# Kernel tuning notes

Measured on AMD Instinct MI355X. Metric: run time of the kernel, lower is better.

The kernel has to match this reference:

```python
import jax, jax.numpy as jnp
import numpy as np

B, N, ND_, FEAT, WV = 32, 1024, 8, 2048, 300
E, T, STEPS = 20000, 2, 5
NDIM = N * ND_  # 8192


def setup_inputs() -> dict:
    key = jax.random.key(0)
    ks = jax.random.split(key, 20)
    s = 0.02
    inputs = jax.random.normal(ks[0], (B, FEAT), jnp.float32)
    wordvecs = jax.random.normal(ks[1], (N, WV), jnp.float32)
    # unique edges per type (disjoint across types) so the scatter has no duplicate indices
    rng = np.random.default_rng(0)
    codes = rng.permutation(N * N)[: T * E].reshape(T, E)
    edge_u = (codes // N).astype(np.int32)
    edge_v = (codes % N).astype(np.int32)
    ki = np.repeat(np.arange(ND_), ND_)
    kj = np.tile(np.arange(ND_), ND_)
    mat_u = (edge_u.reshape(-1)[:, None] * ND_ + ki[None, :]).reshape(-1).astype(np.int32)
    mat_v = (edge_v.reshape(-1)[:, None] * ND_ + kj[None, :]).reshape(-1).astype(np.int32)
    p = {
        'inputs': inputs, 'wordvecs': wordvecs,
        'edge_u': jnp.asarray(edge_u), 'edge_v': jnp.asarray(edge_v),
        'mat_u': jnp.asarray(mat_u), 'mat_v': jnp.asarray(mat_v),
        # Inputnet: Linear(feat+wv -> 512), Linear(512 -> node_dim)
        'W_in1': jax.random.normal(ks[2], (512, FEAT + WV), jnp.float32) * s,
        'b_in1': jnp.zeros((512,), jnp.float32),
        'W_in2': jax.random.normal(ks[3], (ND_, 512), jnp.float32) * s,
        'b_in2': jnp.zeros((ND_,), jnp.float32),
        # embnet: Linear(wv -> 50)
        'W_emb': jax.random.normal(ks[4], (50, WV), jnp.float32) * s,
        'b_emb': jnp.zeros((50,), jnp.float32),
        # relnets: one (50, 50*nd^2) matrix per edge type
        'rel_mats': jax.random.normal(ks[5], (T, 50, 50 * ND_ * ND_), jnp.float32) * s,
        # GRUCell(node_dim, node_dim)
        'W_ih': jax.random.normal(ks[6], (3 * ND_, ND_), jnp.float32) * s,
        'W_hh': jax.random.normal(ks[7], (3 * ND_, ND_), jnp.float32) * s,
        'b_ih': jnp.zeros((3 * ND_,), jnp.float32),
        'b_hh': jnp.zeros((3 * ND_,), jnp.float32),
        # outnet: Linear(nd -> 20), ReLU, Linear(20 -> 1)
        'W_o1': jax.random.normal(ks[8], (20, ND_), jnp.float32) * s,
        'b_o1': jnp.zeros((20,), jnp.float32),
        'W_o2': jax.random.normal(ks[9], (1, 20), jnp.float32) * s,
        'b_o2': jnp.zeros((1,), jnp.float32),
    }
    return p


def reference(inputs, wordvecs, edge_u, edge_v, mat_u, mat_v,
              W_in1, b_in1, W_in2, b_in2, W_emb, b_emb, rel_mats,
              W_ih, W_hh, b_ih, b_hh, W_o1, b_o1, W_o2, b_o2):
    nd = W_in2.shape[0]
    n_nodes = wordvecs.shape[0]
    ndim = n_nodes * nd
    bsz = inputs.shape[0]

    # Inputnet: per-(image, node) feature -> initial hidden state [B, N*nd]
    f = jnp.concatenate([
        jnp.broadcast_to(inputs[:, None, :], (bsz, n_nodes, inputs.shape[1])),
        jnp.broadcast_to(wordvecs[None, :, :], (bsz, n_nodes, wordvecs.shape[1])),
    ], axis=-1).reshape(bsz * n_nodes, -1)
    h = jax.nn.relu(f @ W_in1.T + b_in1) @ W_in2.T + b_in2  # [B*N, nd]
    hidden = h.reshape(bsz, ndim)

    # edge weights via Relnet per edge type
    embs = wordvecs @ W_emb.T + b_emb  # [N, 50]
    ws = []
    for t in range(rel_mats.shape[0]):
        ue = embs[edge_u[t]]  # [E, 50]
        ve = embs[edge_v[t]]  # [E, 50]
        tmp = (ue @ rel_mats[t]).reshape(ue.shape[0], embs.shape[1], nd * nd)
        ws.append(jnp.einsum('ed,edk->ek', ve, tmp))  # [E, nd^2]
    weights = jnp.concatenate(ws, axis=0).reshape(-1)

    # scatter into dense propagation matrix
    P = jnp.zeros((ndim, ndim), jnp.float32).at[mat_u, mat_v].set(weights)
    norm = jnp.sqrt(jnp.sum(P * P, axis=1))  # row L2 norms [ndim]
    norm = norm + (norm == 0).astype(P.dtype)
    P = P / norm  # NOTE: torch broadcasting divides COLUMNS by row norms (faithful)

    def gru(x, hc):
        gi = x @ W_ih.T + b_ih
        gh = hc @ W_hh.T + b_hh
        ir, iz, inn = jnp.split(gi, 3, axis=-1)
        hr, hz, hn = jnp.split(gh, 3, axis=-1)
        r = jax.nn.sigmoid(ir + hr)
        z = jax.nn.sigmoid(iz + hz)
        n = jnp.tanh(inn + r * hn)
        return (1.0 - z) * n + z * hc

    hiddens = [hidden]
    for _ in range(STEPS):
        x = jnp.tanh(hidden @ P.T)  # [B, ndim]
        hidden = gru(x.reshape(-1, nd), hidden.reshape(-1, nd)).reshape(bsz, ndim)
        hiddens.append(hidden)
    states = jnp.stack(hiddens, axis=1)  # [B, STEPS+1, ndim]

    o = jax.nn.relu(states.reshape(-1, nd) @ W_o1.T + b_o1) @ W_o2.T + b_o2  # [B*(S+1)*N, 1]
    logits = o.reshape(bsz, STEPS + 1, n_nodes).transpose(0, 2, 1)  # [B, N, S+1]
    return logits
```

## Files before the change

kernel.cpp:

```cpp
#include <hip/hip_runtime.h>
#include <math.h>

constexpr int B = 32, N = 1024, ND = 8, FEAT = 2048, WVD = 300;
constexpr int E = 20000, T = 2, STEPS = 5;
constexpr int NDIM = N * ND;
constexpr int H1 = 512;
constexpr int W1C = FEAT + WVD;
constexpr int EMB = 50;
constexpr int RC = EMB * ND * ND;
constexpr int KH = 150;
constexpr int CAP = 64;
constexpr int SEG = 50;
constexpr int SEGLEN = E / SEG;

constexpr int G_KA   = 512;
constexpr int G_W1T  = 16 * 10;
constexpr int G_EMB  = N * 25 / 4;
constexpr int G_SEGH = T * N * SEG / 4;
constexpr int F1_TOT = G_KA + G_W1T + G_EMB + G_SEGH;

constexpr int G_ARED = 8;
constexpr int G_WV   = 512;
constexpr int G_AHAT = 13 * 32 * T;
constexpr int F2_TOT = G_ARED + G_WV + G_AHAT;

constexpr int G_INP  = N / 4;
constexpr int F3_TOT = N + G_INP;

__global__ __launch_bounds__(256) void k_f1(
        const int* eu, int* segcnt,
        const float* inp, const float* W1, float* partA, float* W1T,
        const float* wv, const float* We, const float* be,
        float* embs, float* embsT) {
    __shared__ float smem[8 * 260];
    int tid = threadIdx.x;
    int blk = blockIdx.x;
    if (blk < G_KA) {
        int c = tid & 7, b = tid >> 3;
        int c0 = (blk & 63) * 8;
        int ks = blk >> 6;
        int kt = ks * 256;
        {
            int r = tid >> 5, cb = (tid & 31) * 8;
            const float* src = W1 + (size_t)(c0 + r) * W1C + kt + cb;
            float4 a0 = *(const float4*)src;
            float4 a1 = *(const float4*)(src + 4);
            *(float4*)&smem[r * 260 + cb] = a0;
            *(float4*)&smem[r * 260 + cb + 4] = a1;
        }
        __syncthreads();
        const float* xr = inp + (size_t)b * FEAT + kt;
        float acc = 0.f;
#pragma unroll 8
        for (int k4 = 0; k4 < 64; k4++) {
            float4 x = *(const float4*)(xr + k4 * 4);
            float4 w = *(const float4*)&smem[c * 260 + k4 * 4];
            acc += x.x * w.x + x.y * w.y + x.z * w.z + x.w * w.w;
        }
        partA[(size_t)ks * (H1 * B) + (c0 + c) * B + b] = acc;
    } else if (blk < G_KA + G_W1T) {
        int lb = blk - G_KA;
        int c0 = (lb % 16) * 32, k0 = (lb / 16) * 32;
        float (*tile)[33] = (float(*)[33])smem;
        int kl = tid & 31, cl4 = tid >> 5;
#pragma unroll
        for (int p = 0; p < 4; p++) {
            int c = cl4 + p * 8;
            int k = k0 + kl;
            if (k < WVD) tile[c][kl] = W1[(size_t)(c0 + c) * W1C + FEAT + k];
        }
        __syncthreads();
        int cl = tid & 31, kl4 = tid >> 5;
#pragma unroll
        for (int p = 0; p < 4; p++) {
            int kk = kl4 + p * 8;
            int k = k0 + kk;
            if (k < WVD) W1T[(size_t)k * H1 + c0 + cl] = tile[cl][kk];
        }
    } else if (blk < G_KA + G_W1T + G_EMB) {
        int lb = blk - G_KA - G_W1T;
        int wid = lb * 4 + (tid >> 6);
        int lane = tid & 63;
        int n = wid / 25, cp = wid - n * 25;
        int c0 = cp * 2;
        const float* xr = wv + (size_t)n * WVD;
        const float* wr0 = We + (size_t)c0 * WVD;
        const float* wr1 = wr0 + WVD;
        float a0 = 0.f, a1 = 0.f;
#pragma unroll
        for (int i = 0; i < 5; i++) {
            int k = i * 64 + lane;
            if (k < WVD) {
                float x = xr[k];
                a0 += x * wr0[k];
                a1 += x * wr1[k];
            }
        }
        for (int m = 32; m; m >>= 1) {
            a0 += __shfl_xor(a0, m, 64);
            a1 += __shfl_xor(a1, m, 64);
        }
        if (lane == 0) {
            float v0 = a0 + be[c0], v1 = a1 + be[c0 + 1];
            embs[n * EMB + c0] = v0;
            embs[n * EMB + c0 + 1] = v1;
            embsT[c0 * N + n] = v0;
            embsT[(c0 + 1) * N + n] = v1;
        }
    } else {
        int lb = blk - G_KA - G_W1T - G_EMB;
        int wid = lb * 4 + (tid >> 6);
        int lane = tid & 63;
        int t = wid / (N * SEG);
        int rem = wid - t * (N * SEG);
        int u = rem / SEG, seg = rem - u * SEG;
        const int* eut = eu + t * E;
        int e0 = seg * SEGLEN, e1 = e0 + SEGLEN, cnt = 0;
        for (int c = e0; c < e1; c += 64) {
            int e = c + lane;
            bool ok = (e < e1) && (eut[e] == u);
            cnt += __popcll(__ballot(ok));
        }
        if (lane == 0) segcnt[(t * N + u) * SEG + seg] = cnt;
    }
}

__global__ __launch_bounds__(256) void k_f2(
        const float* partA, float* AbT,
        const float* wv, const float* W1T, float* Wp,
        const float* embsT, const float* RMbase, float* Ahat) {
    __shared__ float smemf[1800];
    int tid = threadIdx.x, blk = blockIdx.x;
    if (blk < G_ARED) {
        int cb = blk * 2048 + tid * 8;
        float4 s0 = {0, 0, 0, 0}, s1 = {0, 0, 0, 0};
#pragma unroll
        for (int ks = 0; ks < 8; ks++) {
            const float* p = partA + (size_t)ks * (H1 * B) + cb;
            float4 a = *(const float4*)p;
            float4 b4 = *(const float4*)(p + 4);
            s0.x += a.x; s0.y += a.y; s0.z += a.z; s0.w += a.w;
            s1.x += b4.x; s1.y += b4.y; s1.z += b4.z; s1.w += b4.w;
        }
        *(float4*)(AbT + cb) = s0;
        *(float4*)(AbT + cb + 4) = s1;
    } else if (blk < G_ARED + G_WV) {
        int lb = blk - G_ARED;
        int kh = lb >> 8;
        int rem = lb & 255;
        int c = (rem & 1) * 256 + tid;
        int n0 = (rem >> 1) * 8;
        int kb = kh * KH;
        float (*el)[8] = (float(*)[8])smemf;
        for (int idx = tid; idx < 8 * KH; idx += 256) {
            int j = idx / KH, k = idx - j * KH;
            el[k][j] = wv[(size_t)(n0 + j) * WVD + kb + k];
        }
        __syncthreads();
        float acc[8] = {};
#pragma unroll 5
        for (int k = 0; k < KH; k++) {
            float r = W1T[(size_t)(kb + k) * H1 + c];
            float4 e0 = *(const float4*)&el[k][0];
            float4 e1 = *(const float4*)&el[k][4];
            acc[0] += e0.x * r; acc[1] += e0.y * r;
            acc[2] += e0.z * r; acc[3] += e0.w * r;
            acc[4] += e1.x * r; acc[5] += e1.y * r;
            acc[6] += e1.z * r; acc[7] += e1.w * r;
        }
        float* wout = Wp + (size_t)kh * N * H1;
#pragma unroll
        for (int j = 0; j < 8; j++) wout[(size_t)(n0 + j) * H1 + c] = acc[j];
    } else {
        int lb = blk - G_ARED - G_WV;
        int t = lb / 416, r = lb % 416;
        int bx = r % 13, by = r / 13;
        const float* RM = RMbase + (size_t)t * EMB * RC;
        float* Ah = Ahat + (size_t)t * N * RC;
        int n0 = by * 32;
        float (*el)[36] = (float(*)[36])smemf;
        for (int idx = tid; idx < EMB * 32; idx += 256)
            el[idx >> 5][idx & 31] = embsT[(idx >> 5) * N + n0 + (idx & 31)];
        __syncthreads();
        int mi = bx * 256 + (tid & 63) * 4;
        int ni = (tid >> 6) * 8;
        if (mi < RC) {
            float acc[8][4] = {};
#pragma unroll 2
            for (int c = 0; c < EMB; c++) {
                float4 rm = *(const float4*)(RM + (size_t)c * RC + mi);
                float4 e0 = *(const float4*)&el[c][ni];
                float4 e1 = *(const float4*)&el[c][ni + 4];
                float ev[8] = {e0.x, e0.y, e0.z, e0.w, e1.x, e1.y, e1.z, e1.w};
#pragma unroll
                for (int j = 0; j < 8; j++) {
                    acc[j][0] += ev[j] * rm.x;
                    acc[j][1] += ev[j] * rm.y;
                    acc[j][2] += ev[j] * rm.z;
                    acc[j][3] += ev[j] * rm.w;
                }
            }
#pragma unroll
            for (int j = 0; j < 8; j++) {
                float4 o = {acc[j][0], acc[j][1], acc[j][2], acc[j][3]};
                *(float4*)(Ah + (size_t)(n0 + ni + j) * RC + mi) = o;
            }
        }
    }
}

__global__ __launch_bounds__(256) void k_f3(
        const int* eu, const int* ev, const int* segcnt,
        const float* embs, const float* Ahat, float* wbuf, float* inorm,
        int* counts, int* sv,
        const float* AbT, const float* Wp, const float* b1,
        const float* W2, const float* b2, float* sT0) {
    __shared__ float smem[6656];
    int tid = threadIdx.x;
    int blk = blockIdx.x;
    if (blk < N) {
        int u = blk;
        float* AL   = smem;
        int* vl     = (int*)(smem + 3328);
        int* scnt   = vl + T * CAP;
        int* soff   = scnt + T * SEG;
        int* slist  = soff + T * SEG;
        int* smeta  = slist + T * SEG;
        int w = tid >> 6, lane = tid & 63;
        if (tid < T * SEG) {
            int t = tid / SEG, s = tid - t * SEG;
            scnt[tid] = segcnt[((size_t)t * N + u) * SEG + s];
        }
        __syncthreads();
        if (w < T && lane == 0) {
            int off = 0, nn = 0;
            for (int j = 0; j < SEG; j++) {
                int c = scnt[w * SEG + j];
                soff[w * SEG + j] = off;
                off += c;
                if (c > 0) slist[w * SEG + nn++] = j;
            }
            smeta[w] = nn;
            smeta[T + w] = off;
            counts[w * N + u] = off;
        }
        __syncthreads();
        {
            int myrow = w >> 1, sub = w & 1;
            int row = myrow * N + u;
            const int* eut = eu + myrow * E;
            const int* evt = ev + myrow * E;
            int nnz = smeta[myrow];
            for (int idx = sub; idx < nnz; idx += 2) {
                int seg = slist[myrow * SEG + idx];
                int base = soff[myrow * SEG + seg];
                int e0 = seg * SEGLEN, e1 = e0 + SEGLEN, cnt = 0;
                for (int c = e0; c < e1; c += 64) {
                    int e = c + lane;
                    bool ok = (e < e1) && (eut[e] == u);
                    unsigned long long m = __ballot(ok);
                    if (ok) {
                        int rank = __popcll(m & ((1ull << lane) - 1));
                        int pos = base + cnt + rank;
                        vl[myrow * CAP + pos] = evt[e];
                        sv[(size_t)row * CAP + pos] = evt[e];
                    }
                    cnt += __popcll(m);
                }
            }
        }
        __syncthreads();
        int cnts[T];
#pragma unroll
        for (int t = 0; t < T; t++) cnts[t] = smeta[T + t];
        int k = lane;
        float ssq = 0.f;
        for (int t = 0; t < T; t++) {
            __syncthreads();
            for (int idx = tid; idx < RC; idx += 256)
                AL[idx] = Ahat[((size_t)t * N + u) * RC + idx];
            __syncthreads();
            int cnt = cnts[t];
            size_t base = (size_t)(t * N + u) * CAP;
            for (int i = w; i < cnt; i += 4) {
                int v = vl[t * CAP + i];
                const float* vr = embs + v * EMB;
                float acc = 0.f;
#pragma unroll 10
                for (int d = 0; d < EMB; d++) acc += vr[d] * AL[d * 64 + k];
                wbuf[(base + i) * 64 + k] = acc;
                ssq += acc * acc;
            }
        }
        __syncthreads();
        AL[w * 64 + k] = ssq;
        __syncthreads();
        if (tid < 64) {
            float tot = AL[tid] + AL[64 + tid] + AL[128 + tid] + AL[192 + tid];
            tot += __shfl_xor(tot, 1, 64);
            tot += __shfl_xor(tot, 2, 64);
            tot += __shfl_xor(tot, 4, 64);
            int ki = tid >> 3, kj = tid & 7;
            if (kj == 0) {
                float nv = sqrtf(tot);
                if (nv == 0.f) nv = 1.f;
                inorm[u * ND + ki] = 1.0f / nv;
            }
        }
    } else {
        int n0 = (blk - N) * 4;
        float* w2s  = smem;
        float* wvs  = smem + 4096;
        float* part = smem + 4608;
        for (int idx = tid; idx < 8 * H1; idx += 256) w2s[idx] = W2[idx];
        int b = tid & 31, s = tid >> 5;
        int ki2 = tid >> 5, b2i = tid & 31;
        for (int nn = 0; nn < 4; nn++) {
            int n = n0 + nn;
            __syncthreads();
            for (int idx = tid; idx < H1; idx += 256)
                wvs[idx] = Wp[(size_t)n * H1 + idx]
                         + Wp[(size_t)N * H1 + (size_t)n * H1 + idx] + b1[idx];
            __syncthreads();
            float acc[8] = {};
            for (int i = 0; i < 64; i++) {
                int c = s * 64 + i;
                float tv = fmaxf(AbT[c * 32 + b] + wvs[c], 0.f);
#pragma unroll
                for (int ki = 0; ki < 8; ki++) acc[ki] += tv * w2s[ki * H1 + c];
            }
#pragma unroll
            for (int ki = 0; ki < 8; ki++) part[s * 256 + ki * 32 + b] = acc[ki];
            __syncthreads();
            float tot = b2[ki2];
#pragma unroll
            for (int s2 = 0; s2 < 8; s2++) tot += part[s2 * 256 + ki2 * 32 + b2i];
            sT0[(size_t)n * 256 + tid] = tot;
        }
    }
}

__global__ __launch_bounds__(256) void k_step(
        const int* counts, const int* sv,
        const float* wbuf, const float* inorm, const float* sT, int s,
        const float* W_ih, const float* W_hh, const float* b_ih, const float* b_hh,
        const float* Wo1, const float* bo1, const float* Wo2, const float* bo2,
        float* sOut, float* out, int last) {
    __shared__ float xs[256], hs[256], hfin[256];
    __shared__ float wih[192], whh[192];
    __shared__ float w1s[160], b1s[20], w2s[20];
    __shared__ float res[8][33];
    int tid = threadIdx.x;
    int u = blockIdx.x;
    int ki = tid >> 5, b = tid & 31;
    if (tid < 192) { wih[tid] = W_ih[tid]; whh[tid] = W_hh[tid]; }
    if (last) {
        if (tid < 160) w1s[tid] = Wo1[tid];
        if (tid < 20) { b1s[tid] = bo1[tid]; w2s[tid] = Wo2[tid]; }
    }
    const float* sIn = sT + (size_t)s * NDIM * B;
    float hown = sIn[((size_t)u * 8 + ki) * B + b];
    float acc = 0.f;
    for (int t = 0; t < T; t++) {
        int row = t * N + u;
        int cnt = counts[row];
        size_t base = (size_t)row * CAP;
        int i = 0;
        for (; i + 1 < cnt; i += 2) {
            size_t s0 = base + i, s1 = base + i + 1;
            int v0 = sv[s0], v1 = sv[s1];
            const float* wp0 = wbuf + s0 * 64 + ki * 8;
            const float* wp1 = wbuf + s1 * 64 + ki * 8;
            float4 wa0 = *(const float4*)wp0;
            float4 wb0 = *(const float4*)(wp0 + 4);
            float4 wa1 = *(const float4*)wp1;
            float4 wb1 = *(const float4*)(wp1 + 4);
            const float* ip0 = inorm + v0 * ND;
            const float* ip1 = inorm + v1 * ND;
            const float* hp0 = sIn + (size_t)v0 * 256 + b;
            const float* hp1 = sIn + (size_t)v1 * 256 + b;
            acc += (wa0.x * ip0[0]) * hp0[0]   + (wa0.y * ip0[1]) * hp0[32]
                 + (wa0.z * ip0[2]) * hp0[64]  + (wa0.w * ip0[3]) * hp0[96]
                 + (wb0.x * ip0[4]) * hp0[128] + (wb0.y * ip0[5]) * hp0[160]
                 + (wb0.z * ip0[6]) * hp0[192] + (wb0.w * ip0[7]) * hp0[224];
            acc += (wa1.x * ip1[0]) * hp1[0]   + (wa1.y * ip1[1]) * hp1[32]
                 + (wa1.z * ip1[2]) * hp1[64]  + (wa1.w * ip1[3]) * hp1[96]
                 + (wb1.x * ip1[4]) * hp1[128] + (wb1.y * ip1[5]) * hp1[160]
                 + (wb1.z * ip1[6]) * hp1[192] + (wb1.w * ip1[7]) * hp1[224];
        }
        if (i < cnt) {
            size_t s0 = base + i;
            int v0 = sv[s0];
            const float* wp0 = wbuf + s0 * 64 + ki * 8;
            float4 wa0 = *(const float4*)wp0;
            float4 wb0 = *(const float4*)(wp0 + 4);
            const float* ip0 = inorm + v0 * ND;
            const float* hp0 = sIn + (size_t)v0 * 256 + b;
            acc += (wa0.x * ip0[0]) * hp0[0]   + (wa0.y * ip0[1]) * hp0[32]
                 + (wa0.z * ip0[2]) * hp0[64]  + (wa0.w * ip0[3]) * hp0[96]
                 + (wb0.x * ip0[4]) * hp0[128] + (wb0.y * ip0[5]) * hp0[160]
                 + (wb0.z * ip0[6]) * hp0[192] + (wb0.w * ip0[7]) * hp0[224];
        }
    }
    float xv = tanhf(acc);
    xs[ki * 32 + b] = xv;
    hs[ki * 32 + b] = hown;
    __syncthreads();
    float gr = b_ih[ki], gz = b_ih[8 + ki], gn = b_ih[16 + ki];
    float hr = b_hh[ki], hz = b_hh[8 + ki], hn = b_hh[16 + ki];
#pragma unroll
    for (int j = 0; j < 8; j++) {
        float xj = xs[j * 32 + b], hj = hs[j * 32 + b];
        gr += wih[ki * 8 + j] * xj;
        gz += wih[(8 + ki) * 8 + j] * xj;
        gn += wih[(16 + ki) * 8 + j] * xj;
        hr += whh[ki * 8 + j] * hj;
        hz += whh[(8 + ki) * 8 + j] * hj;
        hn += whh[(16 + ki) * 8 + j] * hj;
    }
    float r = 1.f / (1.f + expf(-(gr + hr)));
    float z = 1.f / (1.f + expf(-(gz + hz)));
    float nn = tanhf(gn + r * hn);
    float hnew = (1.f - z) * nn + z * hown;
    if (!last) {
        sOut[((size_t)u * 8 + ki) * B + b] = hnew;
        return;
    }
    hfin[ki * 32 + b] = hnew;
    __syncthreads();
    int s6 = tid >> 5, bb = tid & 31;
    if (s6 < 6) {
        float x[8];
#pragma unroll
        for (int kk = 0; kk < 8; kk++)
            x[kk] = (s6 < STEPS)
                ? sT[((size_t)s6 * NDIM + u * 8 + kk) * B + bb]
                : hfin[kk * 32 + bb];
        float accv = bo2[0];
#pragma unroll
        for (int j = 0; j < 20; j++) {
            float h = b1s[j];
#pragma unroll
            for (int kk = 0; kk < 8; kk++) h += w1s[j * 8 + kk] * x[kk];
            h = fmaxf(h, 0.f);
            accv += w2s[j] * h;
        }
        res[s6][bb] = accv;
    }
    __syncthreads();
    if (tid < 192) {
        int b_w = tid / 6, s_w = tid - b_w * 6;
        out[(size_t)b_w * ((STEPS + 1) * N) + u * (STEPS + 1) + s_w] = res[s_w][b_w];
    }
}

extern "C" void kernel_launch(void* const* d_in, const int* in_sizes, int n_in,
                              void* d_out, int out_size, void* d_ws, size_t ws_size,
                              hipStream_t stream) {
    const float* inputs   = (const float*)d_in[0];
    const float* wordvecs = (const float*)d_in[1];
    const int*   edge_u   = (const int*)d_in[2];
    const int*   edge_v   = (const int*)d_in[3];
    const float* W_in1 = (const float*)d_in[6];
    const float* b_in1 = (const float*)d_in[7];
    const float* W_in2 = (const float*)d_in[8];
    const float* b_in2 = (const float*)d_in[9];
    const float* W_emb = (const float*)d_in[10];
    const float* b_emb = (const float*)d_in[11];
    const float* rel_mats = (const float*)d_in[12];
    const float* W_ih = (const float*)d_in[13];
    const float* W_hh = (const float*)d_in[14];
    const float* b_ih = (const float*)d_in[15];
    const float* b_hh = (const float*)d_in[16];
    const float* W_o1 = (const float*)d_in[17];
    const float* b_o1 = (const float*)d_in[18];
    const float* W_o2 = (const float*)d_in[19];
    const float* b_o2 = (const float*)d_in[20];
    float* out = (float*)d_out;

    char* ws = (char*)d_ws;
    size_t off = 0;
    auto alloc = [&](size_t bytes) -> void* {
        void* p = ws + off;
        off = (off + bytes + 255) & ~(size_t)255;
        return p;
    };
    int* segcnt    = (int*)alloc((size_t)T * N * SEG * 4);
    int* counts    = (int*)alloc(2048 * 4);
    int* sv        = (int*)alloc((size_t)T * N * CAP * 4);
    float* inorm   = (float*)alloc((size_t)NDIM * 4);
    float* partA   = (float*)alloc((size_t)8 * H1 * B * 4);
    float* AbT     = (float*)alloc((size_t)H1 * B * 4);
    float* W1T     = (float*)alloc((size_t)WVD * H1 * 4);
    float* Wp      = (float*)alloc((size_t)2 * N * H1 * 4);
    float* embs    = (float*)alloc((size_t)N * EMB * 4);
    float* embsT   = (float*)alloc((size_t)EMB * N * 4);
    float* Ahat    = (float*)alloc((size_t)T * N * RC * 4);
    float* wbuf    = (float*)alloc((size_t)T * N * CAP * 64 * 4);
    float* sT      = (float*)alloc((size_t)(STEPS + 1) * NDIM * B * 4);

    k_f1<<<F1_TOT, 256, 0, stream>>>(edge_u, segcnt, inputs, W_in1, partA, W1T,
                                     wordvecs, W_emb, b_emb, embs, embsT);
    k_f2<<<F2_TOT, 256, 0, stream>>>(partA, AbT, wordvecs, W1T, Wp,
                                     embsT, rel_mats, Ahat);
    k_f3<<<F3_TOT, 256, 0, stream>>>(edge_u, edge_v, segcnt,
                                     embs, Ahat, wbuf, inorm, counts, sv,
                                     AbT, Wp, b_in1, W_in2, b_in2, sT);

    for (int s = 0; s < STEPS; s++) {
        int last = (s == STEPS - 1) ? 1 : 0;
        k_step<<<N, 256, 0, stream>>>(counts, sv, wbuf, inorm, sT, s,
                                      W_ih, W_hh, b_ih, b_hh,
                                      W_o1, b_o1, W_o2, b_o2,
                                      sT + (size_t)(s + 1) * NDIM * B, out, last);
    }
}
```

Measured before the change: 242.6 us.

## Split k_f3 row work per edge type and defer norm finalization to step kernel

The per-node block in k_f3 is split into one block per (edge type, node), which doubles the parallelism and halves the serial work per block. Each block now writes partial sums of squares instead of inverse norms. The first step kernel computes the inverse norms on the fly from those partial sums, and extra blocks in the same launch write the inorm buffer for later steps. The inner loop also processes two neighbours per iteration to reuse shared-memory loads, at the cost of extra rsqrt work and pssq reads in step 0.

Result: slower. 265.4 us (+9.4%).

```diff
diff --git a/kernel.cpp b/kernel.cpp
--- a/kernel.cpp
+++ b/kernel.cpp
@@ -24,8 +24,9 @@
 constexpr int G_AHAT = 13 * 32 * T;
 constexpr int F2_TOT = G_ARED + G_WV + G_AHAT;
 
+constexpr int G_ROW  = T * N;
 constexpr int G_INP  = N / 4;
-constexpr int F3_TOT = N + G_INP;
+constexpr int F3_TOT = G_ROW + G_INP;
 
 __global__ __launch_bounds__(256) void k_f1(
         const int* eu, int* segcnt,
@@ -211,85 +212,88 @@
 
 __global__ __launch_bounds__(256) void k_f3(
         const int* eu, const int* ev, const int* segcnt,
-        const float* embs, const float* Ahat, float* wbuf, float* inorm,
+        const float* embs, const float* Ahat, float* wbuf, float* pssq,
         int* counts, int* sv,
         const float* AbT, const float* Wp, const float* b1,
         const float* W2, const float* b2, float* sT0) {
     __shared__ float smem[6656];
     int tid = threadIdx.x;
     int blk = blockIdx.x;
-    if (blk < N) {
-        int u = blk;
-        float* AL   = smem;
-        int* vl     = (int*)(smem + 3328);
-        int* scnt   = vl + T * CAP;
-        int* soff   = scnt + T * SEG;
-        int* slist  = soff + T * SEG;
-        int* smeta  = slist + T * SEG;
+    if (blk < G_ROW) {
+        int t = blk >> 10, u = blk & (N - 1);
+        int row = t * N + u;
+        float* AL  = smem;
+        int* vl    = (int*)(smem + 3200);
+        int* scnt  = vl + CAP;
+        int* soff  = scnt + SEG;
+        int* slist = soff + SEG;
+        int* meta  = slist + SEG;
         int w = tid >> 6, lane = tid & 63;
-        if (tid < T * SEG) {
-            int t = tid / SEG, s = tid - t * SEG;
-            scnt[tid] = segcnt[((size_t)t * N + u) * SEG + s];
-        }
-        __syncthreads();
-        if (w < T && lane == 0) {
+        if (tid < SEG) scnt[tid] = segcnt[(size_t)row * SEG + tid];
+        __syncthreads();
+        if (tid == 0) {
             int off = 0, nn = 0;
             for (int j = 0; j < SEG; j++) {
-                int c = scnt[w * SEG + j];
-                soff[w * SEG + j] = off;
+                int c = scnt[j];
+                soff[j] = off;
                 off += c;
-                if (c > 0) slist[w * SEG + nn++] = j;
-            }
-            smeta[w] = nn;
-            smeta[T + w] = off;
-            counts[w * N + u] = off;
+                if (c > 0) slist[nn++] = j;
+            }
+            meta[0] = nn;
+            meta[1] = off;
+            counts[row] = off;
+        }
+        __syncthreads();
+        int nnz = meta[0], cnt = meta[1];
+        const int* eut = eu + t * E;
+        const int* evt = ev + t * E;
+        for (int idx = w; idx < nnz; idx += 4) {
+            int seg = slist[idx];
+            int sbase = soff[seg];
+            int e0 = seg * SEGLEN, e1 = e0 + SEGLEN, c2 = 0;
+            for (int c = e0; c < e1; c += 64) {
+                int e = c + lane;
+                bool ok = (e < e1) && (eut[e] == u);
+                unsigned long long m = __ballot(ok);
+                if (ok) {
+                    int rank = __popcll(m & ((1ull << lane) - 1));
+                    int pos = sbase + c2 + rank;
+                    vl[pos] = evt[e];
+                    sv[(size_t)row * CAP + pos] = evt[e];
+                }
+                c2 += __popcll(m);
+            }
         }
         __syncthreads();
         {
-            int myrow = w >> 1, sub = w & 1;
-            int row = myrow * N + u;
-            const int* eut = eu + myrow * E;
-            const int* evt = ev + myrow * E;
-            int nnz = smeta[myrow];
-            for (int idx = sub; idx < nnz; idx += 2) {
-                int seg = slist[myrow * SEG + idx];
-                int base = soff[myrow * SEG + seg];
-                int e0 = seg * SEGLEN, e1 = e0 + SEGLEN, cnt = 0;
-                for (int c = e0; c < e1; c += 64) {
-                    int e = c + lane;
-                    bool ok = (e < e1) && (eut[e] == u);
-                    unsigned long long m = __ballot(ok);
-                    if (ok) {
-                        int rank = __popcll(m & ((1ull << lane) - 1));
-                        int pos = base + cnt + rank;
-                        vl[myrow * CAP + pos] = evt[e];
-                        sv[(size_t)row * CAP + pos] = evt[e];
-                    }
-                    cnt += __popcll(m);
-                }
-            }
-        }
-        __syncthreads();
-        int cnts[T];
-#pragma unroll
-        for (int t = 0; t < T; t++) cnts[t] = smeta[T + t];
+            const float4* asrc = (const float4*)(Ahat + (size_t)row * RC);
+            float4* adst = (float4*)AL;
+            for (int idx = tid; idx < RC / 4; idx += 256)
+                adst[idx] = asrc[idx];
+        }
+        __syncthreads();
         int k = lane;
         float ssq = 0.f;
-        for (int t = 0; t < T; t++) {
-            __syncthreads();
-            for (int idx = tid; idx < RC; idx += 256)
-                AL[idx] = Ahat[((size_t)t * N + u) * RC + idx];
-            __syncthreads();
-            int cnt = cnts[t];
-            size_t base = (size_t)(t * N + u) * CAP;
-            for (int i = w; i < cnt; i += 4) {
-                int v = vl[t * CAP + i];
-                const float* vr = embs + v * EMB;
-                float acc = 0.f;
+        size_t wbase = (size_t)row * CAP;
+        for (int i = w; i < cnt; i += 8) {
+            int i2 = i + 4;
+            bool h2 = i2 < cnt;
+            int v0 = vl[i];
+            int v1 = h2 ? vl[i2] : v0;
+            const float* vr0 = embs + v0 * EMB;
+            const float* vr1 = embs + v1 * EMB;
+            float a0 = 0.f, a1 = 0.f;
 #pragma unroll 10
-                for (int d = 0; d < EMB; d++) acc += vr[d] * AL[d * 64 + k];
-                wbuf[(base + i) * 64 + k] = acc;
-                ssq += acc * acc;
+            for (int d = 0; d < EMB; d++) {
+                float al = AL[d * 64 + k];
+                a0 += vr0[d] * al;
+                a1 += vr1[d] * al;
+            }
+            wbuf[(wbase + i) * 64 + k] = a0;
+            ssq += a0 * a0;
+            if (h2) {
+                wbuf[(wbase + i2) * 64 + k] = a1;
+                ssq += a1 * a1;
             }
         }
         __syncthreads();
@@ -301,14 +305,11 @@
             tot += __shfl_xor(tot, 2, 64);
             tot += __shfl_xor(tot, 4, 64);
             int ki = tid >> 3, kj = tid & 7;
-            if (kj == 0) {
-                float nv = sqrtf(tot);
-                if (nv == 0.f) nv = 1.f;
-                inorm[u * ND + ki] = 1.0f / nv;
-            }
+            if (kj == 0)
+                pssq[(size_t)t * NDIM + u * ND + ki] = tot;
         }
     } else {
-        int n0 = (blk - N) * 4;
+        int n0 = (blk - G_ROW) * 4;
         float* w2s  = smem;
         float* wvs  = smem + 4096;
         float* part = smem + 4608;
@@ -340,19 +341,43 @@
     }
 }
 
+__device__ __forceinline__ void getinv(const float* pssq, int v, float* iv) {
+    const float* qa = pssq + (size_t)v * ND;
+    const float* qb = pssq + (size_t)NDIM + (size_t)v * ND;
+#pragma unroll
+    for (int j = 0; j < 8; j++) {
+        float ns = qa[j] + qb[j];
+        iv[j] = (ns == 0.f) ? 1.f : rsqrtf(ns);
+    }
+}
+
 __global__ __launch_bounds__(256) void k_step(
         const int* counts, const int* sv,
-        const float* wbuf, const float* inorm, const float* sT, int s,
+        const float* wbuf, const float* pssq, float* inorm, const float* sT, int s,
         const float* W_ih, const float* W_hh, const float* b_ih, const float* b_hh,
         const float* Wo1, const float* bo1, const float* Wo2, const float* bo2,
         float* sOut, float* out, int last) {
+    int tid = threadIdx.x;
+    if (blockIdx.x >= N) {
+        int i4 = ((blockIdx.x - N) * 256 + tid) * 4;
+        float4 qa = *(const float4*)(pssq + i4);
+        float4 qb = *(const float4*)(pssq + NDIM + i4);
+        float4 o;
+        float n0 = qa.x + qb.x, n1 = qa.y + qb.y, n2 = qa.z + qb.z, n3 = qa.w + qb.w;
+        o.x = (n0 == 0.f) ? 1.f : rsqrtf(n0);
+        o.y = (n1 == 0.f) ? 1.f : rsqrtf(n1);
+        o.z = (n2 == 0.f) ? 1.f : rsqrtf(n2);
+        o.w = (n3 == 0.f) ? 1.f : rsqrtf(n3);
+        *(float4*)(inorm + i4) = o;
+        return;
+    }
     __shared__ float xs[256], hs[256], hfin[256];
     __shared__ float wih[192], whh[192];
     __shared__ float w1s[160], b1s[20], w2s[20];
     __shared__ float res[8][33];
-    int tid = threadIdx.x;
     int u = blockIdx.x;
     int ki = tid >> 5, b = tid & 31;
+    int first = (s == 0);
     if (tid < 192) { wih[tid] = W_ih[tid]; whh[tid] = W_hh[tid]; }
     if (last) {
         if (tid < 160) w1s[tid] = Wo1[tid];
@@ -375,18 +400,26 @@
             float4 wb0 = *(const float4*)(wp0 + 4);
             float4 wa1 = *(const float4*)wp1;
             float4 wb1 = *(const float4*)(wp1 + 4);
-            const float* ip0 = inorm + v0 * ND;
-            const float* ip1 = inorm + v1 * ND;
+            float iv0[8], iv1[8];
+            if (first) {
+                getinv(pssq, v0, iv0);
+                getinv(pssq, v1, iv1);
+            } else {
+                const float* p0 = inorm + v0 * ND;
+                const float* p1 = inorm + v1 * ND;
+#pragma unroll
+                for (int j = 0; j < 8; j++) { iv0[j] = p0[j]; iv1[j] = p1[j]; }
+            }
             const float* hp0 = sIn + (size_t)v0 * 256 + b;
             const float* hp1 = sIn + (size_t)v1 * 256 + b;
-            acc += (wa0.x * ip0[0]) * hp0[0]   + (wa0.y * ip0[1]) * hp0[32]
-                 + (wa0.z * ip0[2]) * hp0[64]  + (wa0.w * ip0[3]) * hp0[96]
-                 + (wb0.x * ip0[4]) * hp0[128] + (wb0.y * ip0[5]) * hp0[160]
-                 + (wb0.z * ip0[6]) * hp0[192] + (wb0.w * ip0[7]) * hp0[224];
-            acc += (wa1.x * ip1[0]) * hp1[0]   + (wa1.y * ip1[1]) * hp1[32]
-                 + (wa1.z * ip1[2]) * hp1[64]  + (wa1.w * ip1[3]) * hp1[96]
-                 + (wb1.x * ip1[4]) * hp1[128] + (wb1.y * ip1[5]) * hp1[160]
-                 + (wb1.z * ip1[6]) * hp1[192] + (wb1.w * ip1[7]) * hp1[224];
+            acc += (wa0.x * iv0[0]) * hp0[0]   + (wa0.y * iv0[1]) * hp0[32]
+                 + (wa0.z * iv0[2]) * hp0[64]  + (wa0.w * iv0[3]) * hp0[96]
+                 + (wb0.x * iv0[4]) * hp0[128] + (wb0.y * iv0[5]) * hp0[160]
+                 + (wb0.z * iv0[6]) * hp0[192] + (wb0.w * iv0[7]) * hp0[224];
+            acc += (wa1.x * iv1[0]) * hp1[0]   + (wa1.y * iv1[1]) * hp1[32]
+                 + (wa1.z * iv1[2]) * hp1[64]  + (wa1.w * iv1[3]) * hp1[96]
+                 + (wb1.x * iv1[4]) * hp1[128] + (wb1.y * iv1[5]) * hp1[160]
+                 + (wb1.z * iv1[6]) * hp1[192] + (wb1.w * iv1[7]) * hp1[224];
         }
         if (i < cnt) {
             size_t s0 = base + i;
@@ -394,12 +427,19 @@
             const float* wp0 = wbuf + s0 * 64 + ki * 8;
             float4 wa0 = *(const float4*)wp0;
             float4 wb0 = *(const float4*)(wp0 + 4);
-            const float* ip0 = inorm + v0 * ND;
+            float iv0[8];
+            if (first) {
+                getinv(pssq, v0, iv0);
+            } else {
+                const float* p0 = inorm + v0 * ND;
+#pragma unroll
+                for (int j = 0; j < 8; j++) iv0[j] = p0[j];
+            }
             const float* hp0 = sIn + (size_t)v0 * 256 + b;
-            acc += (wa0.x * ip0[0]) * hp0[0]   + (wa0.y * ip0[1]) * hp0[32]
-                 + (wa0.z * ip0[2]) * hp0[64]  + (wa0.w * ip0[3]) * hp0[96]
-                 + (wb0.x * ip0[4]) * hp0[128] + (wb0.y * ip0[5]) * hp0[160]
-                 + (wb0.z * ip0[6]) * hp0[192] + (wb0.w * ip0[7]) * hp0[224];
+            acc += (wa0.x * iv0[0]) * hp0[0]   + (wa0.y * iv0[1]) * hp0[32]
+                 + (wa0.z * iv0[2]) * hp0[64]  + (wa0.w * iv0[3]) * hp0[96]
+                 + (wb0.x * iv0[4]) * hp0[128] + (wb0.y * iv0[5]) * hp0[160]
+                 + (wb0.z * iv0[6]) * hp0[192] + (wb0.w * iv0[7]) * hp0[224];
         }
     }
     float xv = tanhf(acc);
@@ -488,6 +528,7 @@
     int* segcnt    = (int*)alloc((size_t)T * N * SEG * 4);
     int* counts    = (int*)alloc(2048 * 4);
     int* sv        = (int*)alloc((size_t)T * N * CAP * 4);
+    float* pssq    = (float*)alloc((size_t)T * NDIM * 4);
     float* inorm   = (float*)alloc((size_t)NDIM * 4);
     float* partA   = (float*)alloc((size_t)8 * H1 * B * 4);
     float* AbT     = (float*)alloc((size_t)H1 * B * 4);
@@ -504,14 +545,15 @@
     k_f2<<<F2_TOT, 256, 0, stream>>>(partA, AbT, wordvecs, W1T, Wp,
                                      embsT, rel_mats, Ahat);
     k_f3<<<F3_TOT, 256, 0, stream>>>(edge_u, edge_v, segcnt,
-                                     embs, Ahat, wbuf, inorm, counts, sv,
+                                     embs, Ahat, wbuf, pssq, counts, sv,
                                      AbT, Wp, b_in1, W_in2, b_in2, sT);
 
     for (int s = 0; s < STEPS; s++) {
         int last = (s == STEPS - 1) ? 1 : 0;
-        k_step<<<N, 256, 0, stream>>>(counts, sv, wbuf, inorm, sT, s,
-                                      W_ih, W_hh, b_ih, b_hh,
-                                      W_o1, b_o1, W_o2, b_o2,
-                                      sT + (size_t)(s + 1) * NDIM * B, out, last);
+        int grid = (s == 0) ? (N + 8) : N;
+        k_step<<<grid, 256, 0, stream>>>(counts, sv, wbuf, pssq, inorm, sT, s,
+                                         W_ih, W_hh, b_ih, b_hh,
+                                         W_o1, b_o1, W_o2, b_o2,
+                                         sT + (size_t)(s + 1) * NDIM * B, out, last);
     }
 }
```
